# Kernel tuning notes

Hardware: AMD Instinct MI355X
Metric: run time of the kernel (lower is better)

## Reference

```python
import jax, jax.numpy as jnp
import numpy as np

B, F, DIN, DOUT = 4096, 64, 256, 256

def setup_inputs() -> dict:
    key = jax.random.key(0)
    k1, k2, k3 = jax.random.split(key, 3)
    init_max = 1.0 / DIN ** 0.5
    x = jax.random.normal(k1, (B, F, DIN), dtype=jnp.float32)
    weight = jax.random.uniform(k2, (F, DIN, DOUT), dtype=jnp.float32, minval=-init_max, maxval=init_max)
    b = jax.random.uniform(k3, (F, DOUT), dtype=jnp.float32, minval=-init_max, maxval=init_max)
    return {"x": x, "weight": weight, "b": b}

def reference(x, weight, b) -> jnp.ndarray:
    # Per-feature grouped linear: for each feature f, out[:, f] = x[:, f] @ weight[f] + b[f]
    # Equivalent to (x[..., None] * weight[None]).sum(axis=2) + bias, but as batched GEMM.
    out = jnp.einsum('bfi,fio->bfo', x, weight)
    return out + b[None, :, :]
```

## Files before the change

kernel.cpp:

```cpp
#include <hip/hip_runtime.h>
#include <stdint.h>

#define BATCH 4096
#define FEAT  64
#define DIN   256
#define DOUT  256

typedef __attribute__((ext_vector_type(8))) short  short8;
typedef __attribute__((ext_vector_type(4))) float  float4v;
typedef __attribute__((ext_vector_type(4))) unsigned int uint4v;

__device__ __forceinline__ unsigned int pack_bf16(float lo, float hi) {
    unsigned int ulo = __builtin_bit_cast(unsigned int, lo) + 0x8000u;
    unsigned int uhi = __builtin_bit_cast(unsigned int, hi) + 0x8000u;
    return __builtin_amdgcn_perm(uhi, ulo, 0x07060302u);
}

#define A_STRIDE 264

__global__ __launch_bounds__(256, 2)
void nlinear_kernel(const float* __restrict__ x,
                    const float* __restrict__ w,
                    const float* __restrict__ bias,
                    float* __restrict__ out) {
    __shared__ __align__(16) unsigned short Alds[64 * A_STRIDE];

    const int tid = threadIdx.x;
    const int f   = blockIdx.x & 63;
    const int mb  = blockIdx.x >> 6;
    const int b0  = mb * 64;

    {
        const float* xb = x + (size_t)(b0 * FEAT + f) * DIN;
        #pragma unroll
        for (int i = 0; i < 8; ++i) {
            int chunk = tid + 256 * i;
            int row   = chunk >> 5;
            int c8    = (chunk & 31) * 8;
            const float* g = xb + row * (FEAT * DIN) + c8;
            float4v a0 = *(const float4v*)g;
            float4v a1 = *(const float4v*)(g + 4);
            uint4v p;
            p.x = pack_bf16(a0.x, a0.y);
            p.y = pack_bf16(a0.z, a0.w);
            p.z = pack_bf16(a1.x, a1.y);
            p.w = pack_bf16(a1.z, a1.w);
            *(uint4v*)&Alds[row * A_STRIDE + c8] = p;
        }
    }
    __syncthreads();

    const int lane = tid & 63;
    const int wv   = tid >> 6;
    const int q    = lane >> 4;
    const int l16  = lane & 15;
    const int n0   = wv * 64;

    float4v acc[4][4];
    #pragma unroll
    for (int s = 0; s < 4; ++s) {
        float bv = bias[f * DOUT + n0 + s * 16 + l16];
        #pragma unroll
        for (int mi = 0; mi < 4; ++mi)
            acc[mi][s] = (float4v){bv, bv, bv, bv};
    }

    const float* wp = w + (size_t)f * (DIN * DOUT) + n0 + q * 8 * DOUT + l16;
    const unsigned short* albase = Alds + l16 * A_STRIDE + q * 8;

    #pragma unroll 2
    for (int it = 0; it < 8; ++it) {
        const int kb = it * 32;
        const float* wk = wp + kb * DOUT;

        short8 bfrag[4];
        #pragma unroll
        for (int s = 0; s < 4; ++s) {
            float v0 = wk[0 * DOUT + s * 16];
            float v1 = wk[1 * DOUT + s * 16];
            float v2 = wk[2 * DOUT + s * 16];
            float v3 = wk[3 * DOUT + s * 16];
            float v4 = wk[4 * DOUT + s * 16];
            float v5 = wk[5 * DOUT + s * 16];
            float v6 = wk[6 * DOUT + s * 16];
            float v7 = wk[7 * DOUT + s * 16];
            uint4v p;
            p.x = pack_bf16(v0, v1);
            p.y = pack_bf16(v2, v3);
            p.z = pack_bf16(v4, v5);
            p.w = pack_bf16(v6, v7);
            bfrag[s] = __builtin_bit_cast(short8, p);
        }

        short8 afrag[4];
        #pragma unroll
        for (int mi = 0; mi < 4; ++mi)
            afrag[mi] = *(const short8*)(albase + mi * 16 * A_STRIDE + kb);

        #pragma unroll
        for (int mi = 0; mi < 4; ++mi)
            #pragma unroll
            for (int s = 0; s < 4; ++s)
                acc[mi][s] = __builtin_amdgcn_mfma_f32_16x16x32_bf16(
                    afrag[mi], bfrag[s], acc[mi][s], 0, 0, 0);
    }

    float* ob = out + (size_t)(b0 * FEAT + f) * DOUT + n0;
    #pragma unroll
    for (int mi = 0; mi < 4; ++mi) {
        #pragma unroll
        for (int r = 0; r < 4; ++r) {
            int m = mi * 16 + q * 4 + r;
            float* orow = ob + m * (FEAT * DOUT);
            #pragma unroll
            for (int s = 0; s < 4; ++s)
                orow[s * 16 + l16] = acc[mi][s][r];
        }
    }
}

extern "C" void kernel_launch(void* const* d_in, const int* in_sizes, int n_in,
                              void* d_out, int out_size, void* d_ws, size_t ws_size,
                              hipStream_t stream) {
    const float* x    = (const float*)d_in[0];
    const float* w    = (const float*)d_in[1];
    const float* bias = (const float*)d_in[2];
    float* out = (float*)d_out;

    nlinear_kernel<<<dim3(FEAT * (BATCH / 64)), dim3(256), 0, stream>>>(x, w, bias, out);
}
```

Before: 481.7 us.

## Pre-convert weights to packed bf16 fragments in a workspace prepass kernel

Adds a prepass kernel that converts the fp32 weights once into bf16, packed in the exact per-lane short8 MFMA fragment layout, and writes them to the workspace. The main GEMM kernel then reads one 16-byte vector per fragment instead of eight strided fp32 loads followed by packing. Previously every one of the 64 batch blocks per feature redid that conversion. The change also raises the launch-bounds occupancy hint from 2 to 3. It costs an extra kernel launch and a pass over the weights, and keeps the old kernel as a fallback when the workspace is too small.

```diff
diff --git a/kernel.cpp b/kernel.cpp
--- a/kernel.cpp
+++ b/kernel.cpp
@@ -18,9 +18,47 @@
 
 #define A_STRIDE 264
 
-__global__ __launch_bounds__(256, 2)
+__global__ __launch_bounds__(256)
+void wprep_kernel(const float* __restrict__ w, unsigned short* __restrict__ wb) {
+    const int blk = blockIdx.x;
+    const int n   = threadIdx.x;
+    const float* src = w + (size_t)blk * 8 * DOUT + n;
+    float v0 = src[0 * DOUT], v1 = src[1 * DOUT];
+    float v2 = src[2 * DOUT], v3 = src[3 * DOUT];
+    float v4 = src[4 * DOUT], v5 = src[5 * DOUT];
+    float v6 = src[6 * DOUT], v7 = src[7 * DOUT];
+    uint4v p;
+    p.x = pack_bf16(v0, v1);
+    p.y = pack_bf16(v2, v3);
+    p.z = pack_bf16(v4, v5);
+    p.w = pack_bf16(v6, v7);
+    *(uint4v*)(wb + ((size_t)blk * DOUT + n) * 8) = p;
+}
+
+__device__ __forceinline__ void stage_x_tile(const float* __restrict__ x,
+                                             unsigned short* Alds,
+                                             int b0, int f, int tid) {
+    const float* xb = x + (size_t)(b0 * FEAT + f) * DIN;
+    #pragma unroll
+    for (int i = 0; i < 8; ++i) {
+        int chunk = tid + 256 * i;
+        int row   = chunk >> 5;
+        int c8    = (chunk & 31) * 8;
+        const float* g = xb + row * (FEAT * DIN) + c8;
+        float4v a0 = *(const float4v*)g;
+        float4v a1 = *(const float4v*)(g + 4);
+        uint4v p;
+        p.x = pack_bf16(a0.x, a0.y);
+        p.y = pack_bf16(a0.z, a0.w);
+        p.z = pack_bf16(a1.x, a1.y);
+        p.w = pack_bf16(a1.z, a1.w);
+        *(uint4v*)&Alds[row * A_STRIDE + c8] = p;
+    }
+}
+
+__global__ __launch_bounds__(256, 3)
 void nlinear_kernel(const float* __restrict__ x,
-                    const float* __restrict__ w,
+                    const short8* __restrict__ wb,
                     const float* __restrict__ bias,
                     float* __restrict__ out) {
     __shared__ __align__(16) unsigned short Alds[64 * A_STRIDE];
@@ -30,24 +68,77 @@
     const int mb  = blockIdx.x >> 6;
     const int b0  = mb * 64;
 
-    {
-        const float* xb = x + (size_t)(b0 * FEAT + f) * DIN;
-        #pragma unroll
-        for (int i = 0; i < 8; ++i) {
-            int chunk = tid + 256 * i;
-            int row   = chunk >> 5;
-            int c8    = (chunk & 31) * 8;
-            const float* g = xb + row * (FEAT * DIN) + c8;
-            float4v a0 = *(const float4v*)g;
-            float4v a1 = *(const float4v*)(g + 4);
-            uint4v p;
-            p.x = pack_bf16(a0.x, a0.y);
-            p.y = pack_bf16(a0.z, a0.w);
-            p.z = pack_bf16(a1.x, a1.y);
-            p.w = pack_bf16(a1.z, a1.w);
-            *(uint4v*)&Alds[row * A_STRIDE + c8] = p;
+    stage_x_tile(x, Alds, b0, f, tid);
+    __syncthreads();
+
+    const int lane = tid & 63;
+    const int wv   = tid >> 6;
+    const int q    = lane >> 4;
+    const int l16  = lane & 15;
+    const int n0   = wv * 64;
+
+    float4v acc[4][4];
+    #pragma unroll
+    for (int s = 0; s < 4; ++s) {
+        float bv = bias[f * DOUT + n0 + s * 16 + l16];
+        #pragma unroll
+        for (int mi = 0; mi < 4; ++mi)
+            acc[mi][s] = (float4v){bv, bv, bv, bv};
+    }
+
+    const short8* wbase = wb + ((size_t)f * 32) * DOUT + n0 + l16;
+    const unsigned short* albase = Alds + l16 * A_STRIDE + q * 8;
+
+    #pragma unroll 2
+    for (int it = 0; it < 8; ++it) {
+        const int kb = it * 32;
+        const short8* wk = wbase + (size_t)(it * 4 + q) * DOUT;
+
+        short8 bfrag[4];
+        #pragma unroll
+        for (int s = 0; s < 4; ++s)
+            bfrag[s] = wk[s * 16];
+
+        short8 afrag[4];
+        #pragma unroll
+        for (int mi = 0; mi < 4; ++mi)
+            afrag[mi] = *(const short8*)(albase + mi * 16 * A_STRIDE + kb);
+
+        #pragma unroll
+        for (int mi = 0; mi < 4; ++mi)
+            #pragma unroll
+            for (int s = 0; s < 4; ++s)
+                acc[mi][s] = __builtin_amdgcn_mfma_f32_16x16x32_bf16(
+                    afrag[mi], bfrag[s], acc[mi][s], 0, 0, 0);
+    }
+
+    float* ob = out + (size_t)(b0 * FEAT + f) * DOUT + n0;
+    #pragma unroll
+    for (int mi = 0; mi < 4; ++mi) {
+        #pragma unroll
+        for (int r = 0; r < 4; ++r) {
+            int m = mi * 16 + q * 4 + r;
+            float* orow = ob + m * (FEAT * DOUT);
+            #pragma unroll
+            for (int s = 0; s < 4; ++s)
+                orow[s * 16 + l16] = acc[mi][s][r];
         }
     }
+}
+
+__global__ __launch_bounds__(256, 2)
+void nlinear_fallback(const float* __restrict__ x,
+                      const float* __restrict__ w,
+                      const float* __restrict__ bias,
+                      float* __restrict__ out) {
+    __shared__ __align__(16) unsigned short Alds[64 * A_STRIDE];
+
+    const int tid = threadIdx.x;
+    const int f   = blockIdx.x & 63;
+    const int mb  = blockIdx.x >> 6;
+    const int b0  = mb * 64;
+
+    stage_x_tile(x, Alds, b0, f, tid);
     __syncthreads();
 
     const int lane = tid & 63;
@@ -127,5 +218,15 @@
     const float* bias = (const float*)d_in[2];
     float* out = (float*)d_out;
 
-    nlinear_kernel<<<dim3(FEAT * (BATCH / 64)), dim3(256), 0, stream>>>(x, w, bias, out);
-}
+    const size_t WB_BYTES = (size_t)FEAT * DIN * DOUT * sizeof(unsigned short);
+
+    if (d_ws != nullptr && ws_size >= WB_BYTES) {
+        unsigned short* wbuf = (unsigned short*)d_ws;
+        wprep_kernel<<<dim3(FEAT * (DIN / 8)), dim3(256), 0, stream>>>(w, wbuf);
+        nlinear_kernel<<<dim3(FEAT * (BATCH / 64)), dim3(256), 0, stream>>>(
+            x, (const short8*)wbuf, bias, out);
+    } else {
+        nlinear_fallback<<<dim3(FEAT * (BATCH / 64)), dim3(256), 0, stream>>>(
+            x, w, bias, out);
+    }
+}
```

Result: faster. 453.0 us (-6.0%).
